# Performance work log

Measured on AMD Instinct MI355X. Metric: run time of the kernel, lower is better.

## Reference

```python
import jax, jax.numpy as jnp
import numpy as np

_OFFS = np.array([(dx, dy, dz) for dx in (-1, 0, 1) for dy in (-1, 0, 1) for dz in (-1, 0, 1)], np.int64)


def setup_inputs() -> dict:
    rng = np.random.default_rng(0)
    B, G, NPTS = 2, 128, 100000
    # level-0 active voxel coords (batch, x, y, z)
    cs = []
    for b in range(B):
        xyz = np.unique(rng.integers(0, G, size=(NPTS, 3)), axis=0)
        cs.append(np.concatenate([np.full((len(xyz), 1), b, np.int64), xyz], 1))
    c0 = np.concatenate(cs, 0)
    c1 = np.unique(np.concatenate([c0[:, :1], c0[:, 1:] // 2], 1), axis=0)  # stride-2 coords
    c2 = np.unique(np.concatenate([c1[:, :1], c1[:, 1:] // 2], 1), axis=0)  # stride-4 coords

    def table(c, g):  # dense coordinate hash: coord -> row index, -1 if empty
        t = np.full((B, g, g, g), -1, np.int64)
        t[c[:, 0], c[:, 1], c[:, 2], c[:, 3]] = np.arange(len(c))
        return t

    t0, t1, t2 = table(c0, G), table(c1, G // 2), table(c2, G // 4)

    def kmap(out_c, tab, g, stride):  # kernel map for k=3 conv: [27, Nout], -1 = no neighbor
        base = out_c[:, 1:] * stride
        nbr = np.empty((27, len(out_c)), np.int32)
        for k, off in enumerate(_OFFS):
            p = base + off
            ok = ((p >= 0) & (p < g)).all(1)
            pc = np.clip(p, 0, g - 1)
            nbr[k] = np.where(ok, tab[out_c[:, 0], pc[:, 0], pc[:, 1], pc[:, 2]], -1)
        return nbr

    nbr0 = kmap(c0, t0, G, 1)        # enc1: submanifold, out coords == in coords
    nbr1 = kmap(c1, t0, G, 2)        # enc2: stride-2 downsample
    nbr2 = kmap(c2, t1, G // 2, 2)   # enc3: stride-2 downsample

    def upmap(fine_c, coarse_tab):   # k=2 s=2 transposed conv: unique parent + offset id
        q = fine_c[:, 1:] // 2
        idx = coarse_tab[fine_c[:, 0], q[:, 0], q[:, 1], q[:, 2]].astype(np.int32)
        r = fine_c[:, 1:] - 2 * q
        off = (r[:, 0] * 4 + r[:, 1] * 2 + r[:, 2]).astype(np.int32)
        return idx, off

    up1_idx, up1_off = upmap(c1, t2)  # dec2: level2 -> level1
    up0_idx, up0_off = upmap(c0, t1)  # dec1: level1 -> level0

    def w(shape):
        return jnp.asarray(rng.normal(0.0, 0.05, shape).astype(np.float32))

    feats = jnp.asarray(rng.normal(0.0, 1.0, (len(c0), 2)).astype(np.float32))
    return dict(
        feats=feats,
        W1=w((27, 2, 32)), W2=w((27, 32, 64)), W3=w((27, 64, 128)),
        W4=w((8, 128, 64)), W5=w((8, 64, 32)), Wout=w((32, 2)),
        g1=jnp.ones(32), b1=jnp.zeros(32), g2=jnp.ones(64), b2=jnp.zeros(64),
        g3=jnp.ones(128), b3=jnp.zeros(128), g4=jnp.ones(64), b4=jnp.zeros(64),
        g5=jnp.ones(32), b5=jnp.zeros(32),
        nbr0=jnp.asarray(nbr0), nbr1=jnp.asarray(nbr1), nbr2=jnp.asarray(nbr2),
        up1_idx=jnp.asarray(up1_idx), up1_off=jnp.asarray(up1_off),
        up0_idx=jnp.asarray(up0_idx), up0_off=jnp.asarray(up0_off),
    )


def _sconv(f, nbr, W):
    # implicit-GEMM sparse conv: gather per kernel offset, matmul, masked accumulate
    out = jnp.zeros((nbr.shape[1], W.shape[2]), f.dtype)
    for k in range(W.shape[0]):
        idx = nbr[k]
        g = jnp.where((idx >= 0)[:, None], f[jnp.maximum(idx, 0)], 0.0)
        out = out + g @ W[k]
    return out


def _upconv(f, pidx, poff, W):
    # k=2 s=2 transposed conv: each fine voxel has exactly one coarse parent + offset id in [0,8)
    g = f[pidx]
    out = jnp.zeros((g.shape[0], W.shape[2]), f.dtype)
    for k in range(8):
        out = out + jnp.where((poff == k)[:, None], g @ W[k], 0.0)
    return out


def _bn_relu(x, g, b):
    # training-mode BatchNorm over the voxel dim (biased var), then ReLU
    mu = x.mean(0)
    var = x.var(0)
    return jax.nn.relu((x - mu) * jax.lax.rsqrt(var + 1e-5) * g + b)


def reference(feats, W1, W2, W3, W4, W5, Wout, g1, b1, g2, b2, g3, b3, g4, b4, g5, b5,
              nbr0, nbr1, nbr2, up1_idx, up1_off, up0_idx, up0_off):
    e1 = _bn_relu(_sconv(feats, nbr0, W1), g1, b1)   # [N0, 32]
    e2 = _bn_relu(_sconv(e1, nbr1, W2), g2, b2)      # [N1, 64]
    e3 = _bn_relu(_sconv(e2, nbr2, W3), g3, b3)      # [N2, 128]
    d2 = _bn_relu(_upconv(e3, up1_idx, up1_off, W4), g4, b4)  # [N1, 64]
    d1 = _bn_relu(_upconv(d2, up0_idx, up0_off, W5), g5, b5)  # [N0, 32]
    return d1 @ Wout                                  # 1x1 conv, [N0, 2]
```

## Files before the change

### kernel.cpp

```cpp
#include <hip/hip_runtime.h>
#include <hip/hip_bf16.h>

typedef __attribute__((ext_vector_type(4))) float  f32x4;
typedef __attribute__((ext_vector_type(8))) short  short8;
typedef __attribute__((ext_vector_type(2))) float  flt2;
typedef long long ll;

__device__ __forceinline__ short f2bf(float f) {
    __hip_bfloat16 h = __float2bfloat16(f);
    short s; __builtin_memcpy(&s, &h, 2);
    return s;
}
__device__ __forceinline__ float bf2f(short s) {
    unsigned u = ((unsigned)(unsigned short)s) << 16;
    float f; __builtin_memcpy(&f, &u, 4);
    return f;
}
__device__ __forceinline__ void gload_lds16(const void* g, void* l) {
    __builtin_amdgcn_global_load_lds(
        (const __attribute__((address_space(1))) unsigned*)(g),
        (__attribute__((address_space(3))) unsigned*)(l),
        16, 0, 0);
}
__device__ __forceinline__ int xcd_swz(int bid, int nwg) {
    int q8 = nwg >> 3, r8 = nwg & 7;
    int xcd = bid & 7, j = bid >> 3;
    return (xcd < r8 ? xcd * (q8 + 1) : r8 * (q8 + 1) + (xcd - r8) * q8) + j;
}

__global__ void prep_kernel(const float* __restrict__ W1, const float* __restrict__ W2,
                            const float* __restrict__ W3, const float* __restrict__ W4,
                            const float* __restrict__ W5,
                            short* W1t, short* W2t, short* W3t, short* W4t, short* W5t) {
    int gid = blockIdx.x * 256 + threadIdx.x;
    if (gid < 32 * 64) {
        int co = gid >> 6, e = gid & 63;
        float v = 0.f;
        if (e < 54) { int k = e >> 1, ci = e & 1; v = W1[(k * 2 + ci) * 32 + co]; }
        W1t[gid] = f2bf(v);
        return;
    }
    int g = gid - 32 * 64;
    if (g < 28 * 2048) { int k = g / 2048, r = g % 2048, co = r >> 5, ci = r & 31;
        W2t[g] = (k < 27) ? f2bf(W2[((ll)k * 32 + ci) * 64 + co]) : (short)0; return; }
    g -= 28 * 2048;
    if (g < 28 * 8192) { int k = g / 8192, r = g % 8192, co = r >> 6, ci = r & 63;
        W3t[g] = (k < 27) ? f2bf(W3[((ll)k * 64 + ci) * 128 + co]) : (short)0; return; }
    g -= 28 * 8192;
    if (g < 8 * 64 * 128) { int k = g / (64*128), r = g % (64*128), co = r >> 7, ci = r & 127;
        W4t[g] = f2bf(W4[((ll)k * 128 + ci) * 64 + co]); return; }
    g -= 8 * 64 * 128;
    if (g < 8 * 32 * 64) { int k = g / (32*64), r = g % (32*64), co = r >> 6, ci = r & 63;
        W5t[g] = f2bf(W5[((ll)k * 64 + ci) * 32 + co]); return; }
}

__launch_bounds__(256)
__global__ void c1_kernel(const float* __restrict__ feats, const int* __restrict__ nbr,
                          const short* __restrict__ W1t, short* __restrict__ out,
                          float* __restrict__ part, int N) {
    __shared__ float sc[8 * 32];
    const int wgid = xcd_swz(blockIdx.x, gridDim.x);
    int tid = threadIdx.x, lane = tid & 63, wave = tid >> 6;
    int rb = wgid * 64 + wave * 16;
    int r = rb + (lane & 15);
    int rl = r < N ? r : N - 1;
    int seg = lane >> 4, l15 = lane & 15;
    f32x4 acc[2];
    acc[0] = (f32x4){0,0,0,0}; acc[1] = (f32x4){0,0,0,0};
    short8 a[2];
    #pragma unroll
    for (int kc = 0; kc < 2; ++kc) {
        #pragma unroll
        for (int j = 0; j < 4; ++j) {
            int k = kc * 16 + seg * 4 + j;
            flt2 f = (flt2){0.f, 0.f};
            if (k < 27) {
                int idx = nbr[(ll)k * N + rl];
                if (idx >= 0) f = *(const flt2*)(feats + 2 * (ll)idx);
            }
            a[kc][2*j]   = f2bf(f[0]);
            a[kc][2*j+1] = f2bf(f[1]);
        }
    }
    #pragma unroll
    for (int kc = 0; kc < 2; ++kc)
        #pragma unroll
        for (int c = 0; c < 2; ++c) {
            short8 b = *(const short8*)(W1t + (c*16 + l15) * 64 + kc * 32 + seg * 8);
            acc[c] = __builtin_amdgcn_mfma_f32_16x16x32_bf16(a[kc], b, acc[c], 0, 0, 0);
        }
    int r0 = rb + seg * 4;
    #pragma unroll
    for (int c = 0; c < 2; ++c) {
        int col = c * 16 + l15;
        #pragma unroll
        for (int j = 0; j < 4; ++j)
            if (r0 + j < N) out[(ll)(r0 + j) * 32 + col] = f2bf(acc[c][j]);
    }
    float s[2], q[2];
    #pragma unroll
    for (int c = 0; c < 2; ++c) { s[c] = 0.f; q[c] = 0.f; }
    #pragma unroll
    for (int c = 0; c < 2; ++c)
        #pragma unroll
        for (int j = 0; j < 4; ++j) {
            float v = (r0 + j < N) ? acc[c][j] : 0.f;
            s[c] += v; q[c] += v * v;
        }
    #pragma unroll
    for (int c = 0; c < 2; ++c) {
        s[c] += __shfl_xor(s[c], 16); q[c] += __shfl_xor(q[c], 16);
        s[c] += __shfl_xor(s[c], 32); q[c] += __shfl_xor(q[c], 32);
    }
    if (lane < 16) {
        #pragma unroll
        for (int c = 0; c < 2; ++c) {
            sc[(wave * 2 + 0) * 32 + c * 16 + l15] = s[c];
            sc[(wave * 2 + 1) * 32 + c * 16 + l15] = q[c];
        }
    }
    __syncthreads();
    for (int i = tid; i < 32; i += 256) {
        float ss = sc[0*32+i] + sc[2*32+i] + sc[4*32+i] + sc[6*32+i];
        float qq = sc[1*32+i] + sc[3*32+i] + sc[5*32+i] + sc[7*32+i];
        part[(ll)wgid * 64 + i]      = ss;
        part[(ll)wgid * 64 + 32 + i] = qq;
    }
}

template<int CIN, int COLS, int RG, int MINW>
__launch_bounds__(256, MINW)
__global__ void msconv7_kernel(const short* __restrict__ inb, const int* __restrict__ nbr,
                               const short* __restrict__ Wt, short* __restrict__ out,
                               float* __restrict__ part, int N, int zoff) {
    constexpr int KC = CIN / 32, NT = COLS / 16;
    constexpr int CPK = COLS * CIN / 8, BIT = CPK / 256;
    constexpr int WST = COLS * CIN;
    constexpr int SH = (CIN == 32) ? 6 : 7;
    __shared__ __align__(16) short lb[2][WST];

    const int wgid = xcd_swz(blockIdx.x, gridDim.x);
    const int tid = threadIdx.x, lane = tid & 63, wave = tid >> 6;
    const int seg = lane >> 4, l15 = lane & 15;
    const int wrb = wgid * (64 * RG) + wave * (16 * RG);
    const char* inB = (const char*)inb;

    int rl[RG];
    #pragma unroll
    for (int rg = 0; rg < RG; ++rg) {
        int r = wrb + rg * 16 + l15;
        rl[rg] = r < N ? r : N - 1;
    }

    auto rawIdx = [&](int k, int (&ix)[RG]) {
        #pragma unroll
        for (int rg = 0; rg < RG; ++rg) ix[rg] = nbr[(ll)k * N + rl[rg]];
    };
    auto mkoff = [&](const int (&ix)[RG], int (&o)[RG]) {
        #pragma unroll
        for (int rg = 0; rg < RG; ++rg) o[rg] = (ix[rg] >= 0) ? (ix[rg] << SH) : zoff;
    };
    auto stage = [&](int kn, int buf) {
        #pragma unroll
        for (int it = 0; it < BIT; ++it) {
            int q = it * 256 + tid;
            int co = q % COLS, sg = (q / COLS) & 3, kc = q / (COLS * 4);
            gload_lds16(Wt + (ll)kn * WST + co * CIN + kc * 32 + sg * 8, &lb[buf][q * 8]);
        }
    };
    auto ldA = [&](short8 (&a)[RG][KC], const int (&o)[RG]) {
        #pragma unroll
        for (int rg = 0; rg < RG; ++rg) {
            const char* base = inB + o[rg];
            #pragma unroll
            for (int kc = 0; kc < KC; ++kc)
                a[rg][kc] = *(const short8*)(base + kc * 64 + seg * 16);
        }
    };

    f32x4 acc[RG][NT];
    #pragma unroll
    for (int rg = 0; rg < RG; ++rg)
        #pragma unroll
        for (int c = 0; c < NT; ++c) acc[rg][c] = (f32x4){0.f, 0.f, 0.f, 0.f};

    auto compute = [&](int buf, short8 (&a)[RG][KC]) {
        #pragma unroll
        for (int kc = 0; kc < KC; ++kc)
            #pragma unroll
            for (int c = 0; c < NT; ++c) {
                short8 b = *(const short8*)&lb[buf][((kc * 4 + seg) * COLS + c * 16 + l15) * 8];
                #pragma unroll
                for (int rg = 0; rg < RG; ++rg)
                    acc[rg][c] = __builtin_amdgcn_mfma_f32_16x16x32_bf16(
                        a[rg][kc], b, acc[rg][c], 0, 0, 0);
            }
    };

    short8 aA[RG][KC], aB[RG][KC];
    int iF[RG], offC[RG];

    {
        int i0[RG], i1[RG], o0[RG];
        rawIdx(0, i0); rawIdx(1, i1); rawIdx(2, iF);
        mkoff(i0, o0); mkoff(i1, offC);
        stage(0, 0);
        __builtin_amdgcn_sched_barrier(0);
        ldA(aA, o0);
        __builtin_amdgcn_sched_barrier(0);
        asm volatile("s_waitcnt vmcnt(%0) lgkmcnt(0)" :: "n"(RG * KC) : "memory");
        __builtin_amdgcn_s_barrier();
        __builtin_amdgcn_sched_barrier(0);
    }

    #pragma unroll
    for (int k = 0; k < 27; ++k) {
        int iN[RG];
        if (k + 1 < 27) {
            if (k + 3 < 27) rawIdx(k + 3, iN);
            __builtin_amdgcn_sched_barrier(0);
            stage(k + 1, (k + 1) & 1);
            __builtin_amdgcn_sched_barrier(0);
            if (k & 1) ldA(aA, offC); else ldA(aB, offC);
            __builtin_amdgcn_sched_barrier(0);
        }
        if (k & 1) compute(1, aB); else compute(0, aA);
        if (k + 1 < 27) {
            __builtin_amdgcn_sched_barrier(0);
            asm volatile("s_waitcnt vmcnt(%0) lgkmcnt(0)" :: "n"(RG * KC) : "memory");
            __builtin_amdgcn_s_barrier();
            __builtin_amdgcn_sched_barrier(0);
            mkoff(iF, offC);
            if (k + 3 < 27) {
                #pragma unroll
                for (int rg = 0; rg < RG; ++rg) iF[rg] = iN[rg];
            }
        }
    }

    #pragma unroll
    for (int rg = 0; rg < RG; ++rg)
        #pragma unroll
        for (int c = 0; c < NT; ++c) {
            int col = c * 16 + l15;
            #pragma unroll
            for (int j = 0; j < 4; ++j) {
                int rr = wrb + rg * 16 + seg * 4 + j;
                if (rr < N) out[(ll)rr * COLS + col] = f2bf(acc[rg][c][j]);
            }
        }

    float s[NT], q[NT];
    #pragma unroll
    for (int c = 0; c < NT; ++c) { s[c] = 0.f; q[c] = 0.f; }
    #pragma unroll
    for (int rg = 0; rg < RG; ++rg)
        #pragma unroll
        for (int c = 0; c < NT; ++c)
            #pragma unroll
            for (int j = 0; j < 4; ++j) {
                int rr = wrb + rg * 16 + seg * 4 + j;
                float v = (rr < N) ? acc[rg][c][j] : 0.f;
                s[c] += v; q[c] += v * v;
            }
    #pragma unroll
    for (int c = 0; c < NT; ++c) {
        s[c] += __shfl_xor(s[c], 16); q[c] += __shfl_xor(q[c], 16);
        s[c] += __shfl_xor(s[c], 32); q[c] += __shfl_xor(q[c], 32);
    }
    __syncthreads();
    float* sc = (float*)&lb[0][0];
    if (lane < 16) {
        #pragma unroll
        for (int c = 0; c < NT; ++c) {
            sc[(wave * 2 + 0) * COLS + c * 16 + l15] = s[c];
            sc[(wave * 2 + 1) * COLS + c * 16 + l15] = q[c];
        }
    }
    __syncthreads();
    for (int i = tid; i < COLS; i += 256) {
        float ss = sc[0*COLS+i] + sc[2*COLS+i] + sc[4*COLS+i] + sc[6*COLS+i];
        float qq = sc[1*COLS+i] + sc[3*COLS+i] + sc[5*COLS+i] + sc[7*COLS+i];
        part[(ll)wgid * 2 * COLS + i]        = ss;
        part[(ll)wgid * 2 * COLS + COLS + i] = qq;
    }
}

__global__ void dcountB_kernel(const int* __restrict__ poffA, int NA, int* __restrict__ cntA,
                               const int* __restrict__ poffB, int NB, int* __restrict__ cntB) {
    const int* poff = blockIdx.y ? poffB : poffA;
    int* cnt = blockIdx.y ? cntB : cntA;
    int N = blockIdx.y ? NB : NA;
    __shared__ int lc[8];
    if (threadIdx.x < 8) lc[threadIdx.x] = 0;
    __syncthreads();
    int r = blockIdx.x * 256 + threadIdx.x;
    if (r < N) atomicAdd(&lc[poff[r]], 1);
    __syncthreads();
    if (threadIdx.x < 8 && lc[threadIdx.x]) atomicAdd(&cnt[threadIdx.x], lc[threadIdx.x]);
}

__global__ void dprefixB_kernel(const int* __restrict__ cntA, int* basesA, int* kofbA,
                                int* permA, int nblkA,
                                const int* __restrict__ cntB, int* basesB, int* kofbB,
                                int* permB, int nblkB) {
    const int* cnt = blockIdx.x ? cntB : cntA;
    int* bases = blockIdx.x ? basesB : basesA;
    int* kofb  = blockIdx.x ? kofbB  : kofbA;
    int* perm  = blockIdx.x ? permB  : permA;
    int nblk   = blockIdx.x ? nblkB  : nblkA;
    __shared__ int base[9];
    if (threadIdx.x == 0) {
        int b = 0;
        for (int k = 0; k < 8; ++k) { base[k] = b; b += (cnt[k] + 63) & ~63; }
        base[8] = b;
        for (int k = 0; k < 9; ++k) bases[k] = base[k];
    }
    __syncthreads();
    int nb = base[8] >> 6;
    for (int i = threadIdx.x; i < nblk; i += 256) {
        int k = -1;
        if (i < nb) {
            int rb = i << 6; k = 0;
            while (rb >= base[k + 1]) ++k;
        }
        kofb[i] = k;
    }
    for (int k = 0; k < 8; ++k) {
        int s = base[k] + cnt[k], e = base[k + 1];
        for (int i = s + threadIdx.x; i < e; i += 256) perm[i] = -1;
    }
}

__global__ void dscatterB_kernel(const int* __restrict__ poffA, const int* basesA,
                                 int* curA, int* permA, int NA,
                                 const int* __restrict__ poffB, const int* basesB,
                                 int* curB, int* permB, int NB) {
    const int* poff = blockIdx.y ? poffB : poffA;
    const int* bases = blockIdx.y ? basesB : basesA;
    int* curp = blockIdx.y ? curB : curA;
    int* perm = blockIdx.y ? permB : permA;
    int N = blockIdx.y ? NB : NA;
    __shared__ int lc[8], lbs[8];
    if (threadIdx.x < 8) lc[threadIdx.x] = 0;
    __syncthreads();
    int r = blockIdx.x * 256 + threadIdx.x;
    int k = 0, myl = 0;
    if (r < N) { k = poff[r]; myl = atomicAdd(&lc[k], 1); }
    __syncthreads();
    if (threadIdx.x < 8) lbs[threadIdx.x] = atomicAdd(&curp[threadIdx.x], lc[threadIdx.x]);
    __syncthreads();
    if (r < N) perm[bases[k] + lbs[k] + myl] = r;
}

template<int CIN, int COUT>
__launch_bounds__(256)
__global__ void gdec_kernel(const short* __restrict__ inb, const int* __restrict__ perm,
                            const int* __restrict__ kofb, const int* __restrict__ pidx,
                            const short* __restrict__ Wt,
                            const float* __restrict__ Abn, const float* __restrict__ Bbn,
                            short* __restrict__ out, float* __restrict__ part) {
    constexpr int KC = CIN / 32, NT = COUT / 16;
    constexpr int CPK = COUT * CIN / 8, BIT = CPK / 256;
    __shared__ __align__(16) short lb[COUT * CIN];
    const int wgid = xcd_swz(blockIdx.x, gridDim.x);
    const int tid = threadIdx.x, lane = tid & 63, wave = tid >> 6;
    int k = kofb[wgid];
    if (k < 0) {
        for (int i = tid; i < 2 * COUT; i += 256) part[(ll)wgid * 2 * COUT + i] = 0.f;
        return;
    }
    const int seg = lane >> 4, l15 = lane & 15;
    const int wrb = wgid * 64 + wave * 16;
    int rl = wrb + l15;
    int pr = perm[rl];
    int idx = pr < 0 ? -1 : pidx[pr];
    int valid = (idx >= 0);

    #pragma unroll
    for (int it = 0; it < BIT; ++it) {
        int q = it * 256 + tid;
        int co = q % COUT, sg = (q / COUT) & 3, kc = q / (COUT * 4);
        gload_lds16(Wt + ((ll)k * COUT + co) * CIN + kc * 32 + sg * 8, &lb[q * 8]);
    }
    f32x4 cA[KC][2], cB[KC][2];
    #pragma unroll
    for (int kc = 0; kc < KC; ++kc) {
        cA[kc][0] = *(const f32x4*)(Abn + kc * 32 + seg * 8);
        cA[kc][1] = *(const f32x4*)(Abn + kc * 32 + seg * 8 + 4);
        cB[kc][0] = *(const f32x4*)(Bbn + kc * 32 + seg * 8);
        cB[kc][1] = *(const f32x4*)(Bbn + kc * 32 + seg * 8 + 4);
    }
    short8 a[KC];
    const short* base = inb + (ll)(idx < 0 ? 0 : idx) * CIN;
    #pragma unroll
    for (int kc = 0; kc < KC; ++kc) {
        short8 raw = *(const short8*)(base + kc * 32 + seg * 8);
        #pragma unroll
        for (int j = 0; j < 8; ++j) {
            float x = bf2f(raw[j]);
            float y = fmaf(x, cA[kc][j >> 2][j & 3], cB[kc][j >> 2][j & 3]);
            y = y > 0.f ? y : 0.f;
            a[kc][j] = valid ? f2bf(y) : (short)0;
        }
    }

    f32x4 acc[NT];
    #pragma unroll
    for (int c = 0; c < NT; ++c) acc[c] = (f32x4){0.f, 0.f, 0.f, 0.f};
    __syncthreads();
    #pragma unroll
    for (int kc = 0; kc < KC; ++kc)
        #pragma unroll
        for (int c = 0; c < NT; ++c) {
            short8 b = *(const short8*)&lb[((kc * 4 + seg) * COUT + c * 16 + l15) * 8];
            acc[c] = __builtin_amdgcn_mfma_f32_16x16x32_bf16(a[kc], b, acc[c], 0, 0, 0);
        }
    #pragma unroll
    for (int j = 0; j < 4; ++j) {
        int prs = __shfl(pr, seg * 4 + j, 64);
        if (prs >= 0) {
            #pragma unroll
            for (int c = 0; c < NT; ++c)
                out[(ll)prs * COUT + c * 16 + l15] = f2bf(acc[c][j]);
        }
    }
    float s[NT], q[NT];
    #pragma unroll
    for (int c = 0; c < NT; ++c) { s[c] = 0.f; q[c] = 0.f; }
    #pragma unroll
    for (int c = 0; c < NT; ++c)
        #pragma unroll
        for (int j = 0; j < 4; ++j) { float v = acc[c][j]; s[c] += v; q[c] += v * v; }
    #pragma unroll
    for (int c = 0; c < NT; ++c) {
        s[c] += __shfl_xor(s[c], 16); q[c] += __shfl_xor(q[c], 16);
        s[c] += __shfl_xor(s[c], 32); q[c] += __shfl_xor(q[c], 32);
    }
    __syncthreads();
    float* sc = (float*)lb;
    if (lane < 16) {
        #pragma unroll
        for (int c = 0; c < NT; ++c) {
            sc[(wave * 2 + 0) * COUT + c * 16 + l15] = s[c];
            sc[(wave * 2 + 1) * COUT + c * 16 + l15] = q[c];
        }
    }
    __syncthreads();
    for (int i = tid; i < COUT; i += 256) {
        float ss = sc[0*COUT+i] + sc[2*COUT+i] + sc[4*COUT+i] + sc[6*COUT+i];
        float qq = sc[1*COUT+i] + sc[3*COUT+i] + sc[5*COUT+i] + sc[7*COUT+i];
        part[(ll)wgid * 2 * COUT + i]        = ss;
        part[(ll)wgid * 2 * COUT + COUT + i] = qq;
    }
}

__global__ void red2_kernel(const float* __restrict__ part, int nblk,
                            const float* __restrict__ g, const float* __restrict__ bb,
                            float* __restrict__ A, float* __restrict__ B, int C, int N) {
    int c = blockIdx.x;
    float s = 0.f, q = 0.f;
    for (int i = threadIdx.x; i < nblk; i += 256) {
        s += part[(ll)i * 2 * C + c];
        q += part[(ll)i * 2 * C + C + c];
    }
    __shared__ float ls[256], lq[256];
    ls[threadIdx.x] = s; lq[threadIdx.x] = q;
    __syncthreads();
    for (int str = 128; str >= 1; str >>= 1) {
        if (threadIdx.x < str) {
            ls[threadIdx.x] += ls[threadIdx.x + str];
            lq[threadIdx.x] += lq[threadIdx.x + str];
        }
        __syncthreads();
    }
    if (threadIdx.x == 0) {
        float inv = 1.0f / (float)N;
        float mu = ls[0] * inv, var = lq[0] * inv - mu * mu;
        float a = g[c] * rsqrtf(var + 1e-5f);
        A[c] = a; B[c] = bb[c] - mu * a;
    }
}

template<int C>
__global__ void bnrelu_kernel(const short* __restrict__ x, const float* __restrict__ A,
                              const float* __restrict__ B, short* __restrict__ out, int N) {
    constexpr int CPR = C / 8;
    int i = blockIdx.x * 256 + threadIdx.x;
    if (i >= N * CPR) return;
    int r = i / CPR, ch = i - r * CPR;
    short8 v = *(const short8*)(x + (ll)r * C + ch * 8);
    short8 o;
    #pragma unroll
    for (int j = 0; j < 8; ++j) {
        int c = ch * 8 + j;
        float y = fmaf(bf2f(v[j]), A[c], B[c]);
        o[j] = f2bf(y > 0.f ? y : 0.f);
    }
    *(short8*)(out + (ll)r * C + ch * 8) = o;
}

__global__ void outk_kernel(const short* __restrict__ z, const float* __restrict__ A,
                            const float* __restrict__ B, const float* __restrict__ Wout,
                            float* __restrict__ out, int N) {
    __shared__ float w[64], sa[32], sb[32];
    if (threadIdx.x < 64) w[threadIdx.x] = Wout[threadIdx.x];
    if (threadIdx.x < 32) { sa[threadIdx.x] = A[threadIdx.x]; sb[threadIdx.x] = B[threadIdx.x]; }
    __syncthreads();
    int r = blockIdx.x * 256 + threadIdx.x;
    if (r >= N) return;
    const short* zp = z + (ll)r * 32;
    float o0 = 0.f, o1 = 0.f;
    #pragma unroll
    for (int s4 = 0; s4 < 4; ++s4) {
        short8 v = *(const short8*)(zp + s4 * 8);
        #pragma unroll
        for (int j = 0; j < 8; ++j) {
            int c = s4 * 8 + j;
            float y = fmaf(bf2f(v[j]), sa[c], sb[c]);
            y = y > 0.f ? y : 0.f;
            o0 = fmaf(y, w[2*c], o0);
            o1 = fmaf(y, w[2*c+1], o1);
        }
    }
    out[(ll)r * 2]     = o0;
    out[(ll)r * 2 + 1] = o1;
}

extern "C" void kernel_launch(void* const* d_in, const int* in_sizes, int n_in,
                              void* d_out, int out_size, void* d_ws, size_t ws_size,
                              hipStream_t stream) {
    const float* feats = (const float*)d_in[0];
    const float* W1 = (const float*)d_in[1];
    const float* W2 = (const float*)d_in[2];
    const float* W3 = (const float*)d_in[3];
    const float* W4 = (const float*)d_in[4];
    const float* W5 = (const float*)d_in[5];
    const float* Wout = (const float*)d_in[6];
    const float* g1 = (const float*)d_in[7],  *b1 = (const float*)d_in[8];
    const float* g2 = (const float*)d_in[9],  *b2 = (const float*)d_in[10];
    const float* g3 = (const float*)d_in[11], *b3 = (const float*)d_in[12];
    const float* g4 = (const float*)d_in[13], *b4 = (const float*)d_in[14];
    const float* g5 = (const float*)d_in[15], *b5 = (const float*)d_in[16];
    const int* nbr0 = (const int*)d_in[17];
    const int* nbr1 = (const int*)d_in[18];
    const int* nbr2 = (const int*)d_in[19];
    const int* up1_idx = (const int*)d_in[20];
    const int* up1_off = (const int*)d_in[21];
    const int* up0_idx = (const int*)d_in[22];
    const int* up0_off = (const int*)d_in[23];

    const int N0 = in_sizes[0] / 2;
    const int N1 = in_sizes[20];
    const int N2 = in_sizes[19] / 27;

    char* cur = (char*)d_ws;
    auto alloc = [&](size_t bytes) { char* p = cur; cur += (bytes + 255) & ~255ULL; return p; };
    auto cdiv = [](ll a, ll b) { return (int)((a + b - 1) / b); };

    float* stats = (float*)alloc(4096);
    float* A1 = stats,       *B1c = stats + 32;
    float* A2 = stats + 64,  *B2c = stats + 128;
    float* A3 = stats + 192, *B3c = stats + 320;
    float* A4 = stats + 448, *B4c = stats + 512;
    float* A5 = stats + 576, *B5c = stats + 608;
    short* zrow  = (short*)((char*)stats + 2560);
    int*   cnt4  = (int*)((char*)stats + 3072);
    int*   cur4  = (int*)((char*)stats + 3104);
    int*   cnt5  = (int*)((char*)stats + 3136);
    int*   cur5  = (int*)((char*)stats + 3168);
    int*   bas4  = (int*)((char*)stats + 3200);
    int*   bas5  = (int*)((char*)stats + 3264);

    float* part = (float*)alloc(2 * 1024 * 1024);

    short* z1  = (short*)alloc((size_t)N0 * 32 * 2);
    short* e1b = (short*)alloc((size_t)N0 * 32 * 2);
    short* z2  = (short*)alloc((size_t)N1 * 64 * 2);
    short* e2b = (short*)alloc((size_t)N1 * 64 * 2);
    short* z3  = (short*)alloc((size_t)N2 * 128 * 2);
    short* z4  = (short*)alloc((size_t)N1 * 64 * 2);
    short* z5  = (short*)alloc((size_t)N0 * 32 * 2);
    short* W1t = (short*)alloc(32 * 64 * 2);
    short* W2t = (short*)alloc((size_t)28 * 64 * 32 * 2);
    short* W3t = (short*)alloc((size_t)28 * 128 * 64 * 2);
    short* W4t = (short*)alloc((size_t)8 * 64 * 128 * 2);
    short* W5t = (short*)alloc((size_t)8 * 32 * 64 * 2);

    const int gridL4 = cdiv((ll)N1 + 512, 64);
    const int gridL5 = cdiv((ll)N0 + 512, 64);
    int* perm4 = (int*)alloc((size_t)gridL4 * 64 * 4);
    int* kofb4 = (int*)alloc((size_t)gridL4 * 4);
    int* perm5 = (int*)alloc((size_t)gridL5 * 64 * 4);
    int* kofb5 = (int*)alloc((size_t)gridL5 * 4);

    const int zoff1 = (int)((ll)((char*)zrow - (char*)e1b));
    const int zoff2 = (int)((ll)((char*)zrow - (char*)e2b));

    const int nblk1 = cdiv(N0, 64);
    const int nblk2 = cdiv(N1, 128);
    const int nblk3 = cdiv(N2, 64);

    hipMemsetAsync((char*)stats + 2560, 0, 640, stream);

    prep_kernel<<<cdiv(2048 + 28*2048 + 28*8192 + 65536 + 16384, 256), 256, 0, stream>>>(
        W1, W2, W3, W4, W5, W1t, W2t, W3t, W4t, W5t);

    {
        int gx = cdiv(N1 > N0 ? N1 : N0, 256);
        dcountB_kernel<<<dim3(gx, 2), 256, 0, stream>>>(up1_off, N1, cnt4, up0_off, N0, cnt5);
        dprefixB_kernel<<<2, 256, 0, stream>>>(cnt4, bas4, kofb4, perm4, gridL4,
                                               cnt5, bas5, kofb5, perm5, gridL5);
        dscatterB_kernel<<<dim3(gx, 2), 256, 0, stream>>>(up1_off, bas4, cur4, perm4, N1,
                                                          up0_off, bas5, cur5, perm5, N0);
    }

    c1_kernel<<<nblk1, 256, 0, stream>>>(feats, nbr0, W1t, z1, part, N0);
    red2_kernel<<<32, 256, 0, stream>>>(part, nblk1, g1, b1, A1, B1c, 32, N0);
    bnrelu_kernel<32><<<cdiv((ll)N0 * 4, 256), 256, 0, stream>>>(z1, A1, B1c, e1b, N0);

    msconv7_kernel<32, 64, 2, 4><<<nblk2, 256, 0, stream>>>(e1b, nbr1, W2t, z2, part, N1, zoff1);
    red2_kernel<<<64, 256, 0, stream>>>(part, nblk2, g2, b2, A2, B2c, 64, N1);
    bnrelu_kernel<64><<<cdiv((ll)N1 * 8, 256), 256, 0, stream>>>(z2, A2, B2c, e2b, N1);

    msconv7_kernel<64, 128, 1, 3><<<nblk3, 256, 0, stream>>>(e2b, nbr2, W3t, z3, part, N2, zoff2);
    red2_kernel<<<128, 256, 0, stream>>>(part, nblk3, g3, b3, A3, B3c, 128, N2);

    gdec_kernel<128, 64><<<gridL4, 256, 0, stream>>>(z3, perm4, kofb4, up1_idx, W4t, A3, B3c, z4, part);
    red2_kernel<<<64, 256, 0, stream>>>(part, gridL4, g4, b4, A4, B4c, 64, N1);

    gdec_kernel<64, 32><<<gridL5, 256, 0, stream>>>(z4, perm5, kofb5, up0_idx, W5t, A4, B4c, z5, part);
    red2_kernel<<<32, 256, 0, stream>>>(part, gridL5, g5, b5, A5, B5c, 32, N0);

    outk_kernel<<<cdiv(N0, 256), 256, 0, stream>>>(z5, A5, B5c, Wout, (float*)d_out, N0);
}
```

Before: 256.6 us.

## Add full-weight-in-LDS kernel for level-2 conv and double rows per wave for level-3

Adds a specialized enc2 sparse conv kernel that loads all 27 weight slices (about 108KB) into LDS once, prefetches neighbor indices into registers and keeps an 8-deep ring of gathered activation loads ahead of the MFMAs. This replaces the double-buffered weight streaming of the generic kernel. It costs occupancy, since the kernel runs at one workgroup per CU with heavy register use. The enc3 conv now processes two row-groups per wave, halving the grid and raising weight reuse, at the cost of fewer blocks on a small level.

After: 258.2 us. No clear change (+0.6%).

```diff
diff --git a/kernel.cpp b/kernel.cpp
--- a/kernel.cpp
+++ b/kernel.cpp
@@ -125,6 +125,122 @@
         float qq = sc[1*32+i] + sc[3*32+i] + sc[5*32+i] + sc[7*32+i];
         part[(ll)wgid * 64 + i]      = ss;
         part[(ll)wgid * 64 + 32 + i] = qq;
+    }
+}
+
+__launch_bounds__(256, 1)
+__global__ void msL2full_kernel(const short* __restrict__ inb, const int* __restrict__ nbr,
+                                const short* __restrict__ Wt, short* __restrict__ out,
+                                float* __restrict__ part, int N, int zoff) {
+    constexpr int RG = 2;
+    __shared__ __align__(16) short lb[27 * 2048];
+
+    const int wgid = xcd_swz(blockIdx.x, gridDim.x);
+    const int tid = threadIdx.x, lane = tid & 63, wave = tid >> 6;
+    const int seg = lane >> 4, l15 = lane & 15;
+    const int wrb = wgid * 128 + wave * 32;
+    const char* inB = (const char*)inb;
+
+    int rl[RG];
+    #pragma unroll
+    for (int rg = 0; rg < RG; ++rg) {
+        int r = wrb + rg * 16 + l15;
+        rl[rg] = r < N ? r : N - 1;
+    }
+
+    {
+        int co = tid & 63, sg = tid >> 6;
+        #pragma unroll
+        for (int it = 0; it < 27; ++it)
+            gload_lds16(Wt + (ll)it * 2048 + co * 32 + sg * 8, &lb[it * 2048 + tid * 8]);
+    }
+
+    int off[27][RG];
+    #pragma unroll
+    for (int k = 0; k < 27; ++k)
+        #pragma unroll
+        for (int rg = 0; rg < RG; ++rg) {
+            int idx = nbr[(ll)k * N + rl[rg]];
+            off[k][rg] = (idx >= 0) ? (idx << 6) : zoff;
+        }
+
+    auto ldA = [&](short8 (&a)[RG], const int (&o)[RG]) {
+        #pragma unroll
+        for (int rg = 0; rg < RG; ++rg)
+            a[rg] = *(const short8*)(inB + o[rg] + seg * 16);
+    };
+
+    short8 aR[8][RG];
+    #pragma unroll
+    for (int p = 0; p < 8; ++p) ldA(aR[p], off[p]);
+
+    asm volatile("s_waitcnt vmcnt(0) lgkmcnt(0)" ::: "memory");
+    __builtin_amdgcn_s_barrier();
+
+    f32x4 acc[RG][4];
+    #pragma unroll
+    for (int rg = 0; rg < RG; ++rg)
+        #pragma unroll
+        for (int c = 0; c < 4; ++c) acc[rg][c] = (f32x4){0.f, 0.f, 0.f, 0.f};
+
+    #pragma unroll
+    for (int k = 0; k < 27; ++k) {
+        #pragma unroll
+        for (int c = 0; c < 4; ++c) {
+            short8 b = *(const short8*)&lb[k * 2048 + (seg * 64 + c * 16 + l15) * 8];
+            #pragma unroll
+            for (int rg = 0; rg < RG; ++rg)
+                acc[rg][c] = __builtin_amdgcn_mfma_f32_16x16x32_bf16(
+                    aR[k & 7][rg], b, acc[rg][c], 0, 0, 0);
+        }
+        if (k + 8 < 27) ldA(aR[k & 7], off[k + 8]);
+    }
+
+    #pragma unroll
+    for (int rg = 0; rg < RG; ++rg)
+        #pragma unroll
+        for (int c = 0; c < 4; ++c) {
+            int col = c * 16 + l15;
+            #pragma unroll
+            for (int j = 0; j < 4; ++j) {
+                int rr = wrb + rg * 16 + seg * 4 + j;
+                if (rr < N) out[(ll)rr * 64 + col] = f2bf(acc[rg][c][j]);
+            }
+        }
+
+    float s[4], q[4];
+    #pragma unroll
+    for (int c = 0; c < 4; ++c) { s[c] = 0.f; q[c] = 0.f; }
+    #pragma unroll
+    for (int rg = 0; rg < RG; ++rg)
+        #pragma unroll
+        for (int c = 0; c < 4; ++c)
+            #pragma unroll
+            for (int j = 0; j < 4; ++j) {
+                int rr = wrb + rg * 16 + seg * 4 + j;
+                float v = (rr < N) ? acc[rg][c][j] : 0.f;
+                s[c] += v; q[c] += v * v;
+            }
+    #pragma unroll
+    for (int c = 0; c < 4; ++c) {
+        s[c] += __shfl_xor(s[c], 16); q[c] += __shfl_xor(q[c], 16);
+        s[c] += __shfl_xor(s[c], 32); q[c] += __shfl_xor(q[c], 32);
+    }
+    __syncthreads();
+    float* sc = (float*)&lb[0];
+    if (lane < 16) {
+        #pragma unroll
+        for (int c = 0; c < 4; ++c) {
+            sc[(wave * 2 + 0) * 64 + c * 16 + l15] = s[c];
+            sc[(wave * 2 + 1) * 64 + c * 16 + l15] = q[c];
+        }
+    }
+    __syncthreads();
+    for (int i = tid; i < 64; i += 256) {
+        float ss = sc[0*64+i] + sc[2*64+i] + sc[4*64+i] + sc[6*64+i];
+        float qq = sc[1*64+i] + sc[3*64+i] + sc[5*64+i] + sc[7*64+i];
+        part[(ll)wgid * 128 + i]      = ss;
+        part[(ll)wgid * 128 + 64 + i] = qq;
     }
 }
 
@@ -599,7 +715,7 @@
 
     const int nblk1 = cdiv(N0, 64);
     const int nblk2 = cdiv(N1, 128);
-    const int nblk3 = cdiv(N2, 64);
+    const int nblk3 = cdiv(N2, 128);
 
     hipMemsetAsync((char*)stats + 2560, 0, 640, stream);
 
@@ -619,11 +735,11 @@
     red2_kernel<<<32, 256, 0, stream>>>(part, nblk1, g1, b1, A1, B1c, 32, N0);
     bnrelu_kernel<32><<<cdiv((ll)N0 * 4, 256), 256, 0, stream>>>(z1, A1, B1c, e1b, N0);
 
-    msconv7_kernel<32, 64, 2, 4><<<nblk2, 256, 0, stream>>>(e1b, nbr1, W2t, z2, part, N1, zoff1);
+    msL2full_kernel<<<nblk2, 256, 0, stream>>>(e1b, nbr1, W2t, z2, part, N1, zoff1);
     red2_kernel<<<64, 256, 0, stream>>>(part, nblk2, g2, b2, A2, B2c, 64, N1);
     bnrelu_kernel<64><<<cdiv((ll)N1 * 8, 256), 256, 0, stream>>>(z2, A2, B2c, e2b, N1);
 
-    msconv7_kernel<64, 128, 1, 3><<<nblk3, 256, 0, stream>>>(e2b, nbr2, W3t, z3, part, N2, zoff2);
+    msconv7_kernel<64, 128, 2, 3><<<nblk3, 256, 0, stream>>>(e2b, nbr2, W3t, z3, part, N2, zoff2);
     red2_kernel<<<128, 256, 0, stream>>>(part, nblk3, g3, b3, A3, B3c, 128, N2);
 
     gdec_kernel<128, 64><<<gridL4, 256, 0, stream>>>(z3, perm4, kofb4, up1_idx, W4t, A3, B3c, z4, part);
```
